# Performance work log

Hardware: AMD Instinct MI355X
Metric: run time of the kernel (lower is better)

Reference implementation:

```python
import jax, jax.numpy as jnp
import numpy as np

D, H, F, E, K = 1024, 16, 2048, 8, 2
EPS = 1e-5


def layernorm(x, g, b):
    m = jnp.mean(x, axis=-1, keepdims=True)
    v = jnp.mean((x - m) ** 2, axis=-1, keepdims=True)
    return (x - m) * jax.lax.rsqrt(v + EPS) * g + b


def mha(q_in, k_in, v_in, wq, wk, wv, bq, bk, bv, wo, bo):
    B, Tq, Dm = q_in.shape
    Tk = k_in.shape[1]
    dh = Dm // H
    q = (q_in @ wq + bq).reshape(B, Tq, H, dh)
    k = (k_in @ wk + bk).reshape(B, Tk, H, dh)
    v = (v_in @ wv + bv).reshape(B, Tk, H, dh)
    scores = jnp.einsum('bqhd,bkhd->bhqk', q, k) / jnp.sqrt(jnp.asarray(dh, q.dtype))
    attn = jax.nn.softmax(scores, axis=-1)
    out = jnp.einsum('bhqk,bkhd->bqhd', attn, v).reshape(B, Tq, Dm)
    return out @ wo + bo


def moe(x, rw, rb, w1, b1, w2, b2):
    B, T, Dm = x.shape
    xt = x.reshape(-1, Dm)                      # [N, D]
    N = xt.shape[0]
    logits = xt @ rw + rb                       # [N, E]
    probs = jax.nn.softmax(logits, axis=-1)
    topv, topi = jax.lax.top_k(probs, K)        # [N, K]
    gates = topv / jnp.sum(topv, axis=-1, keepdims=True)
    dense_gates = jnp.zeros((N, E), x.dtype).at[jnp.arange(N)[:, None], topi].set(gates)
    h = jax.nn.relu(jnp.einsum('td,edf->etf', xt, w1) + b1[:, None, :])  # [E, N, F]
    y = jnp.einsum('etf,efd->etd', h, w2) + b2[:, None, :]               # [E, N, D]
    out = jnp.einsum('te,etd->td', dense_gates, y).reshape(B, T, Dm)
    frac = jnp.mean(jnp.sum(jax.nn.one_hot(topi, E, dtype=x.dtype), axis=1) / K, axis=0)  # [E]
    importance = jnp.mean(probs, axis=0)        # [E]
    lb_loss = E * jnp.sum(frac * importance)
    return out, lb_loss


def forward(tgt, memory,
            sa_wq, sa_wk, sa_wv, sa_bq, sa_bk, sa_bv, sa_wo, sa_bo,
            ca_wq, ca_wk, ca_wv, ca_bq, ca_bk, ca_bv, ca_wo, ca_bo,
            ln1_g, ln1_b, ln2_g, ln2_b, ln3_g, ln3_b,
            rw, rb, w1, b1, w2, b2):
    t2 = mha(tgt, tgt, tgt, sa_wq, sa_wk, sa_wv, sa_bq, sa_bk, sa_bv, sa_wo, sa_bo)
    t = layernorm(tgt + t2, ln1_g, ln1_b)
    t2 = mha(t, memory, memory, ca_wq, ca_wk, ca_wv, ca_bq, ca_bk, ca_bv, ca_wo, ca_bo)
    t = layernorm(t + t2, ln2_g, ln2_b)
    t2, lb = moe(t, rw, rb, w1, b1, w2, b2)
    t = layernorm(t + t2, ln3_g, ln3_b)
    return t, lb


def setup_inputs() -> dict:
    key = jax.random.key(0)
    ks = jax.random.split(key, 24)
    s = 1.0 / np.sqrt(D)
    inp = {
        'tgt': jax.random.normal(ks[0], (4, 512, D), jnp.float32),
        'memory': jax.random.normal(ks[1], (4, 512, D), jnp.float32),
    }
    names = ['sa_wq', 'sa_wk', 'sa_wv', 'sa_wo', 'ca_wq', 'ca_wk', 'ca_wv', 'ca_wo']
    for i, n in enumerate(names):
        inp[n] = jax.random.normal(ks[2 + i], (D, D), jnp.float32) * s
    for n in ['sa_bq', 'sa_bk', 'sa_bv', 'sa_bo', 'ca_bq', 'ca_bk', 'ca_bv', 'ca_bo']:
        inp[n] = jnp.zeros((D,), jnp.float32)
    for n in ['ln1_g', 'ln2_g', 'ln3_g']:
        inp[n] = jnp.ones((D,), jnp.float32)
    for n in ['ln1_b', 'ln2_b', 'ln3_b']:
        inp[n] = jnp.zeros((D,), jnp.float32)
    inp['rw'] = jax.random.normal(ks[10], (D, E), jnp.float32) * s
    inp['rb'] = jnp.zeros((E,), jnp.float32)
    inp['w1'] = jax.random.normal(ks[11], (E, D, F), jnp.float32) * s
    inp['b1'] = jnp.zeros((E, F), jnp.float32)
    inp['w2'] = jax.random.normal(ks[12], (E, F, D), jnp.float32) * (1.0 / np.sqrt(F))
    inp['b2'] = jnp.zeros((E, D), jnp.float32)
    return inp


def reference(tgt, memory,
              sa_wq, sa_wk, sa_wv, sa_bq, sa_bk, sa_bv, sa_wo, sa_bo,
              ca_wq, ca_wk, ca_wv, ca_bq, ca_bk, ca_bv, ca_wo, ca_bo,
              ln1_g, ln1_b, ln2_g, ln2_b, ln3_g, ln3_b,
              rw, rb, w1, b1, w2, b2):
    return forward(tgt, memory,
                   sa_wq, sa_wk, sa_wv, sa_bq, sa_bk, sa_bv, sa_wo, sa_bo,
                   ca_wq, ca_wk, ca_wv, ca_bq, ca_bk, ca_bv, ca_wo, ca_bo,
                   ln1_g, ln1_b, ln2_g, ln2_b, ln3_g, ln3_b,
                   rw, rb, w1, b1, w2, b2)
```

## Files before the change

kernel.cpp:

```cpp
#include <hip/hip_runtime.h>

constexpr int Dm = 1024;
constexpr int NH = 16;
constexpr int Ff = 2048;
constexpr int NE = 8;
constexpr int Bn = 4;
constexpr int Tn = 512;
constexpr int Nt = 2048;

typedef float  f32x4  __attribute__((ext_vector_type(4)));
typedef __bf16 bf16x8 __attribute__((ext_vector_type(8)));
typedef unsigned short u16;
typedef u16 u16x8v __attribute__((ext_vector_type(8)));
typedef u16 u16x4v __attribute__((ext_vector_type(4)));

__device__ inline u16 f2bf(float f) {
    unsigned u = __builtin_bit_cast(unsigned, f);
    u += 0x7FFFu + ((u >> 16) & 1u);
    return (u16)(u >> 16);
}
__device__ inline float bf2f(u16 h) {
    unsigned u = (unsigned)h << 16;
    return __builtin_bit_cast(float, u);
}
__device__ inline void splitbf(float x, u16& hi, u16& lo) {
    hi = f2bf(x);
    lo = f2bf(x - bf2f(hi));
}
__device__ inline bf16x8 ld_frag(const u16* p) {
    return __builtin_bit_cast(bf16x8, *(const u16x8v*)p);
}
__device__ inline void cp16(const u16* g, u16* l) {
    __builtin_amdgcn_global_load_lds(
        (const __attribute__((address_space(1))) unsigned int*)g,
        (__attribute__((address_space(3))) unsigned int*)l, 16, 0, 0);
}

template <int SPLIT, int CMODE>
__global__ __launch_bounds__(256) void gemm_kernel(
    const u16* __restrict__ Ahi, const u16* __restrict__ Alo, int lda,
    const u16* __restrict__ Whi, const u16* __restrict__ Wlo, size_t weStride,
    const float* __restrict__ B0, const float* __restrict__ B1,
    const float* __restrict__ B2, size_t beStride,
    void* __restrict__ C0, void* __restrict__ C1, int ldc,
    int Mparam, int K,
    const int* __restrict__ lst, int lstStride, const int* __restrict__ cnt,
    int mode, int relu,
    const u16* __restrict__ A2hi, const u16* __restrict__ A2lo, int lda2,
    const u16* __restrict__ W2hi, const u16* __restrict__ W2lo,
    const float* __restrict__ B20, const float* __restrict__ B21,
    void* __restrict__ C20, void* __restrict__ C21, int ldc2, int xSplit,
    const float* __restrict__ gatep, float* __restrict__ accOut)
{
    __shared__ __align__(16) u16 AsH[128 * 32];
    __shared__ __align__(16) u16 WsH[128 * 32];
    __shared__ __align__(16) u16 AsL[SPLIT ? 128 * 32 : 8];
    __shared__ __align__(16) u16 WsL[SPLIT ? 128 * 32 : 8];
    __shared__ int inIdx[128];
    __shared__ int outIdx[128];

    const int e = blockIdx.z;
    const int M = (mode == 0) ? Mparam : cnt[e];
    const int m0 = blockIdx.y * 128;
    if (m0 >= M) return;

    int bx = blockIdx.x;
    const u16 *aH = Ahi, *aL = Alo, *wH = Whi, *wL = Wlo;
    const float *b0 = B0, *b1 = B1, *b2 = B2;
    void *c0 = C0, *c1 = C1;
    int myLda = lda, myLdc = ldc;
    if (xSplit && bx >= xSplit) {
        bx -= xSplit;
        aH = A2hi; aL = A2lo; wH = W2hi; wL = W2lo;
        b0 = B20; b1 = B21; b2 = B21;
        c0 = C20; c1 = C21; myLda = lda2; myLdc = ldc2;
    }
    const int n0 = bx * 128;
    const int seg = n0 >> 10, nseg = n0 & 1023;
    const float* bias = ((seg == 0) ? b0 : (seg == 1) ? b1 : b2) + (size_t)e * beStride;
    const int tid = threadIdx.x;

    if (tid < 128) {
        int g = m0 + tid;
        bool valid = g < M;
        int gi, go;
        if (mode == 0) { gi = valid ? g : (M - 1); go = valid ? g : -1; }
        else {
            int pid = lst[(size_t)e * lstStride + (valid ? g : 0)];
            gi = (mode == 1) ? (pid >> 1) : pid;
            go = valid ? pid : -1;
        }
        inIdx[tid] = gi;
        outIdx[tid] = go;
    }
    __syncthreads();

    const int lane = tid & 63, wv = tid >> 6;
    const int c0i = wv * 2, c1i = wv * 2 + 1;
    const int r0 = c0i * 16 + (lane >> 2), r1 = c1i * 16 + (lane >> 2);
    const int kc0 = (lane & 3) ^ ((r0 >> 1) & 3);
    const int kc1 = (lane & 3) ^ ((r1 >> 1) & 3);
    const size_t wOff = (size_t)e * weStride;
    const u16* aH0 = aH + (size_t)inIdx[r0] * myLda + kc0 * 8;
    const u16* aH1 = aH + (size_t)inIdx[r1] * myLda + kc1 * 8;
    const u16* wH0 = wH + wOff + (size_t)(n0 + r0) * K + kc0 * 8;
    const u16* wH1 = wH + wOff + (size_t)(n0 + r1) * K + kc1 * 8;
    const u16 *aL0 = nullptr, *aL1 = nullptr, *wL0 = nullptr, *wL1 = nullptr;
    if (SPLIT) {
        aL0 = aL + (size_t)inIdx[r0] * myLda + kc0 * 8;
        aL1 = aL + (size_t)inIdx[r1] * myLda + kc1 * 8;
        wL0 = wL + wOff + (size_t)(n0 + r0) * K + kc0 * 8;
        wL1 = wL + wOff + (size_t)(n0 + r1) * K + kc1 * 8;
    }
    u16* ldsA0 = &AsH[c0i * 512];
    u16* ldsA1 = &AsH[c1i * 512];
    u16* ldsW0 = &WsH[c0i * 512];
    u16* ldsW1 = &WsH[c1i * 512];
    u16* ldsAL0 = SPLIT ? &AsL[c0i * 512] : nullptr;
    u16* ldsAL1 = SPLIT ? &AsL[c1i * 512] : nullptr;
    u16* ldsWL0 = SPLIT ? &WsL[c0i * 512] : nullptr;
    u16* ldsWL1 = SPLIT ? &WsL[c1i * 512] : nullptr;

    const int wy = (wv >> 1) * 64, wx = (wv & 1) * 64;
    const int l15 = lane & 15, quad = lane >> 4;

    f32x4 acc[4][4];
    #pragma unroll
    for (int i = 0; i < 4; ++i)
        #pragma unroll
        for (int j = 0; j < 4; ++j) acc[i][j] = (f32x4)0.f;

    for (int k0 = 0; k0 < K; k0 += 32) {
        cp16(aH0 + k0, ldsA0);
        cp16(aH1 + k0, ldsA1);
        cp16(wH0 + k0, ldsW0);
        cp16(wH1 + k0, ldsW1);
        if (SPLIT) {
            cp16(aL0 + k0, ldsAL0);
            cp16(aL1 + k0, ldsAL1);
            cp16(wL0 + k0, ldsWL0);
            cp16(wL1 + k0, ldsWL1);
        }
        __syncthreads();

        bf16x8 ah[4], bh[4], al[4], bl[4];
        #pragma unroll
        for (int mi = 0; mi < 4; ++mi) {
            int r = wy + mi * 16 + l15;
            int sl = quad ^ ((r >> 1) & 3);
            ah[mi] = ld_frag(&AsH[r * 32 + sl * 8]);
            if (SPLIT) al[mi] = ld_frag(&AsL[r * 32 + sl * 8]);
        }
        #pragma unroll
        for (int ni = 0; ni < 4; ++ni) {
            int r = wx + ni * 16 + l15;
            int sl = quad ^ ((r >> 1) & 3);
            bh[ni] = ld_frag(&WsH[r * 32 + sl * 8]);
            if (SPLIT) bl[ni] = ld_frag(&WsL[r * 32 + sl * 8]);
        }
        #pragma unroll
        for (int mi = 0; mi < 4; ++mi)
            #pragma unroll
            for (int ni = 0; ni < 4; ++ni) {
                acc[mi][ni] = __builtin_amdgcn_mfma_f32_16x16x32_bf16(
                    ah[mi], bh[ni], acc[mi][ni], 0, 0, 0);
                if (SPLIT) {
                    acc[mi][ni] = __builtin_amdgcn_mfma_f32_16x16x32_bf16(
                        ah[mi], bl[ni], acc[mi][ni], 0, 0, 0);
                    acc[mi][ni] = __builtin_amdgcn_mfma_f32_16x16x32_bf16(
                        al[mi], bh[ni], acc[mi][ni], 0, 0, 0);
                }
            }
        __syncthreads();
    }

    #pragma unroll
    for (int mi = 0; mi < 4; ++mi) {
        #pragma unroll
        for (int r = 0; r < 4; ++r) {
            int rl = wy + mi * 16 + quad * 4 + r;
            int orow = outIdx[rl];
            if (orow < 0) continue;
            #pragma unroll
            for (int ni = 0; ni < 4; ++ni) {
                int col = nseg + wx + ni * 16 + l15;
                float val = acc[mi][ni][r] + bias[col];
                if (relu) val = fmaxf(val, 0.f);
                int gcol = n0 + wx + ni * 16 + l15;
                if (CMODE == 3) {
                    atomicAdd(&accOut[(size_t)(orow >> 1) * Dm + gcol],
                              gatep[orow] * val);
                } else if (CMODE == 2) {
                    u16 hh, ll;
                    splitbf(val, hh, ll);
                    ((u16*)c0)[(size_t)orow * myLdc + gcol] = hh;
                    ((u16*)c1)[(size_t)orow * myLdc + gcol] = ll;
                } else if (CMODE == 1) {
                    ((u16*)c0)[(size_t)orow * myLdc + gcol] = f2bf(val);
                } else {
                    ((float*)c0)[(size_t)orow * myLdc + gcol] = val;
                }
            }
        }
    }
}

__global__ __launch_bounds__(256) void attn_kernel(
    const u16* __restrict__ QH, const u16* __restrict__ QL, int qld, int qOff,
    const u16* __restrict__ KH, const u16* __restrict__ KL, int kld, int kOff,
    const u16* __restrict__ VH, const u16* __restrict__ VL, int vld, int vOff,
    u16* __restrict__ OH, u16* __restrict__ OL)
{
    __shared__ __align__(16) u16 KtH[64 * 72], KtL[64 * 72];
    __shared__ __align__(16) u16 VtH[64 * 72], VtL[64 * 72];
    __shared__ __align__(16) u16 PtH[4][16 * 72], PtL[4][16 * 72];

    const int tid = threadIdx.x, lane = tid & 63, wv = tid >> 6;
    const int quad = lane >> 4, l15 = lane & 15;
    const int b = blockIdx.z, h = blockIdx.y, q0 = blockIdx.x * 64;
    const int bT = b * Tn;

    bf16x8 aqh[2], aql[2];
    {
        size_t qbase = (size_t)(bT + q0 + wv * 16 + l15) * qld + qOff + h * 64;
        #pragma unroll
        for (int s = 0; s < 2; ++s) {
            aqh[s] = ld_frag(QH + qbase + s * 32 + quad * 8);
            aql[s] = ld_frag(QL + qbase + s * 32 + quad * 8);
        }
    }

    f32x4 oacc[4];
    #pragma unroll
    for (int i = 0; i < 4; ++i) oacc[i] = (f32x4)0.f;
    float mrow[4] = {-1e30f, -1e30f, -1e30f, -1e30f};
    float lrow[4] = {0.f, 0.f, 0.f, 0.f};

    const int rr = tid >> 2, cc = tid & 3;

    for (int kt0 = 0; kt0 < Tn; kt0 += 64) {
        {
            size_t kb = (size_t)(bT + kt0 + rr) * kld + kOff + h * 64 + cc * 16;
            *(u16x8v*)&KtH[rr * 72 + cc * 16]     = *(const u16x8v*)(KH + kb);
            *(u16x8v*)&KtH[rr * 72 + cc * 16 + 8] = *(const u16x8v*)(KH + kb + 8);
            *(u16x8v*)&KtL[rr * 72 + cc * 16]     = *(const u16x8v*)(KL + kb);
            *(u16x8v*)&KtL[rr * 72 + cc * 16 + 8] = *(const u16x8v*)(KL + kb + 8);

            size_t vb = (size_t)(bT + kt0 + rr) * vld + vOff + h * 64 + cc * 16;
            u16x8v va = *(const u16x8v*)(VH + vb);
            u16x8v vbv = *(const u16x8v*)(VH + vb + 8);
            u16x8v la = *(const u16x8v*)(VL + vb);
            u16x8v lb = *(const u16x8v*)(VL + vb + 8);
            #pragma unroll
            for (int i = 0; i < 8; ++i) {
                VtH[(cc * 16 + i) * 72 + rr]     = va[i];
                VtH[(cc * 16 + 8 + i) * 72 + rr] = vbv[i];
                VtL[(cc * 16 + i) * 72 + rr]     = la[i];
                VtL[(cc * 16 + 8 + i) * 72 + rr] = lb[i];
            }
        }
        __syncthreads();

        f32x4 sacc[4];
        #pragma unroll
        for (int nt = 0; nt < 4; ++nt) {
            sacc[nt] = (f32x4)0.f;
            #pragma unroll
            for (int s = 0; s < 2; ++s) {
                bf16x8 bkh = ld_frag(&KtH[(nt * 16 + l15) * 72 + s * 32 + quad * 8]);
                bf16x8 bkl = ld_frag(&KtL[(nt * 16 + l15) * 72 + s * 32 + quad * 8]);
                sacc[nt] = __builtin_amdgcn_mfma_f32_16x16x32_bf16(aqh[s], bkh, sacc[nt], 0, 0, 0);
                sacc[nt] = __builtin_amdgcn_mfma_f32_16x16x32_bf16(aqh[s], bkl, sacc[nt], 0, 0, 0);
                sacc[nt] = __builtin_amdgcn_mfma_f32_16x16x32_bf16(aql[s], bkh, sacc[nt], 0, 0, 0);
            }
        }
        #pragma unroll
        for (int nt = 0; nt < 4; ++nt)
            #pragma unroll
            for (int r = 0; r < 4; ++r) sacc[nt][r] *= 0.125f;

        float alpha[4], mnew[4];
        #pragma unroll
        for (int r = 0; r < 4; ++r) {
            float mx = fmaxf(fmaxf(sacc[0][r], sacc[1][r]), fmaxf(sacc[2][r], sacc[3][r]));
            #pragma unroll
            for (int msk = 1; msk < 16; msk <<= 1) mx = fmaxf(mx, __shfl_xor(mx, msk));
            mnew[r] = fmaxf(mrow[r], mx);
            alpha[r] = __expf(mrow[r] - mnew[r]);
            mrow[r] = mnew[r];
        }
        float rs[4] = {0.f, 0.f, 0.f, 0.f};
        #pragma unroll
        for (int nt = 0; nt < 4; ++nt)
            #pragma unroll
            for (int r = 0; r < 4; ++r) {
                float p = __expf(sacc[nt][r] - mnew[r]);
                sacc[nt][r] = p;
                rs[r] += p;
            }
        #pragma unroll
        for (int r = 0; r < 4; ++r) {
            #pragma unroll
            for (int msk = 1; msk < 16; msk <<= 1) rs[r] += __shfl_xor(rs[r], msk);
            lrow[r] = lrow[r] * alpha[r] + rs[r];
        }
        #pragma unroll
        for (int ni = 0; ni < 4; ++ni)
            #pragma unroll
            for (int r = 0; r < 4; ++r) oacc[ni][r] *= alpha[r];

        #pragma unroll
        for (int nt = 0; nt < 4; ++nt)
            #pragma unroll
            for (int r = 0; r < 4; ++r) {
                u16 hh, ll;
                splitbf(sacc[nt][r], hh, ll);
                PtH[wv][(quad * 4 + r) * 72 + nt * 16 + l15] = hh;
                PtL[wv][(quad * 4 + r) * 72 + nt * 16 + l15] = ll;
            }
        asm volatile("s_waitcnt lgkmcnt(0)" ::: "memory");

        #pragma unroll
        for (int s = 0; s < 2; ++s) {
            bf16x8 aph = ld_frag(&PtH[wv][l15 * 72 + s * 32 + quad * 8]);
            bf16x8 apl = ld_frag(&PtL[wv][l15 * 72 + s * 32 + quad * 8]);
            #pragma unroll
            for (int ni = 0; ni < 4; ++ni) {
                bf16x8 bvh = ld_frag(&VtH[(ni * 16 + l15) * 72 + s * 32 + quad * 8]);
                bf16x8 bvl = ld_frag(&VtL[(ni * 16 + l15) * 72 + s * 32 + quad * 8]);
                oacc[ni] = __builtin_amdgcn_mfma_f32_16x16x32_bf16(aph, bvh, oacc[ni], 0, 0, 0);
                oacc[ni] = __builtin_amdgcn_mfma_f32_16x16x32_bf16(aph, bvl, oacc[ni], 0, 0, 0);
                oacc[ni] = __builtin_amdgcn_mfma_f32_16x16x32_bf16(apl, bvh, oacc[ni], 0, 0, 0);
            }
        }
        __syncthreads();
    }

    #pragma unroll
    for (int r = 0; r < 4; ++r) {
        float inv = 1.f / lrow[r];
        int orow = bT + q0 + wv * 16 + quad * 4 + r;
        #pragma unroll
        for (int ni = 0; ni < 4; ++ni) {
            int col = h * 64 + ni * 16 + l15;
            u16 hh, ll;
            splitbf(oacc[ni][r] * inv, hh, ll);
            OH[(size_t)orow * Dm + col] = hh;
            OL[(size_t)orow * Dm + col] = ll;
        }
    }
}

__global__ __launch_bounds__(256) void ln_residual_kernel(
    const float* __restrict__ X, const float* __restrict__ R,
    const float* __restrict__ g, const float* __restrict__ bta,
    float* __restrict__ Out, u16* __restrict__ outH, u16* __restrict__ outL)
{
    __shared__ float red[8];
    const int t = blockIdx.x, tid = threadIdx.x;
    float v[4];
    float s = 0.f;
    #pragma unroll
    for (int i = 0; i < 4; ++i) {
        int c = tid + i * 256;
        v[i] = X[(size_t)t * Dm + c] + R[(size_t)t * Dm + c];
        s += v[i];
    }
    #pragma unroll
    for (int off = 32; off; off >>= 1) s += __shfl_down(s, off);
    const int wid = tid >> 6;
    if ((tid & 63) == 0) red[wid] = s;
    __syncthreads();
    const float mean = (red[0] + red[1] + red[2] + red[3]) * (1.f / 1024.f);
    float s2 = 0.f;
    #pragma unroll
    for (int i = 0; i < 4; ++i) { float d = v[i] - mean; s2 += d * d; }
    #pragma unroll
    for (int off = 32; off; off >>= 1) s2 += __shfl_down(s2, off);
    if ((tid & 63) == 0) red[4 + wid] = s2;
    __syncthreads();
    const float var  = (red[4] + red[5] + red[6] + red[7]) * (1.f / 1024.f);
    const float rstd = rsqrtf(var + 1e-5f);
    #pragma unroll
    for (int i = 0; i < 4; ++i) {
        int c = tid + i * 256;
        float o = (v[i] - mean) * rstd * g[c] + bta[c];
        Out[(size_t)t * Dm + c] = o;
        if (outH) {
            u16 hh, ll;
            splitbf(o, hh, ll);
            outH[(size_t)t * Dm + c] = hh;
            outL[(size_t)t * Dm + c] = ll;
        }
    }
}

__global__ __launch_bounds__(256) void split_kernel(
    const float* __restrict__ src, u16* __restrict__ hi, u16* __restrict__ lo)
{
    int i = (blockIdx.x * 256 + threadIdx.x) * 4;
    float4 v = *(const float4*)(src + i);
    u16x4v h, l;
    u16 hh, ll;
    splitbf(v.x, hh, ll); h[0] = hh; l[0] = ll;
    splitbf(v.y, hh, ll); h[1] = hh; l[1] = ll;
    splitbf(v.z, hh, ll); h[2] = hh; l[2] = ll;
    splitbf(v.w, hh, ll); h[3] = hh; l[3] = ll;
    *(u16x4v*)(hi + i) = h;
    *(u16x4v*)(lo + i) = l;
}

__global__ __launch_bounds__(256) void wT_kernel(
    const float* __restrict__ src, size_t srcEStride, int Ksrc, int Nsrc,
    u16* __restrict__ dhi, u16* __restrict__ dlo, size_t dstEStride)
{
    __shared__ float tile[64][65];
    const int e = blockIdx.z;
    src += (size_t)e * srcEStride;
    dhi += (size_t)e * dstEStride;
    if (dlo) dlo += (size_t)e * dstEStride;
    const int n0 = blockIdx.x * 64, k0 = blockIdx.y * 64;
    for (int i = threadIdx.x; i < 4096; i += 256) {
        int r = i >> 6, c = i & 63;
        tile[r][c] = src[(size_t)(k0 + r) * Nsrc + n0 + c];
    }
    __syncthreads();
    for (int i = threadIdx.x; i < 4096; i += 256) {
        int r = i >> 6, c = i & 63;
        float v = tile[c][r];
        u16 hh, ll;
        splitbf(v, hh, ll);
        dhi[(size_t)(n0 + r) * Ksrc + k0 + c] = hh;
        if (dlo) dlo[(size_t)(n0 + r) * Ksrc + k0 + c] = ll;
    }
}

constexpr int RT_TPB = 32;
__global__ __launch_bounds__(256) void router_kernel(
    const float* __restrict__ X, const float* __restrict__ rw,
    const float* __restrict__ rb, float* __restrict__ gatep,
    int* __restrict__ elist, int* __restrict__ ecnt,
    float* __restrict__ impf, float* __restrict__ cntf)
{
    __shared__ float simp[NE];
    __shared__ int   scnt[NE];
    __shared__ int   sbase[NE];
    __shared__ int   sexp[RT_TPB][2];
    __shared__ int   spos[RT_TPB][2];

    const int tid = threadIdx.x, lane = tid & 63, wv = tid >> 6;
    if (tid < NE) { simp[tid] = 0.f; scnt[tid] = 0; }
    __syncthreads();

    const int t0 = blockIdx.x * RT_TPB;

    for (int i = 0; i < 8; ++i) {
        const int slot = wv * 8 + i;
        const int t = t0 + slot;
        float l[NE];
        #pragma unroll
        for (int e = 0; e < NE; ++e) l[e] = 0.f;
        #pragma unroll
        for (int j = 0; j < Dm / 64; ++j) {
            int d = lane + j * 64;
            float x = X[(size_t)t * Dm + d];
            #pragma unroll
            for (int e = 0; e < NE; ++e) l[e] += x * rw[d * NE + e];
        }
        #pragma unroll
        for (int e = 0; e < NE; ++e) {
            float vv = l[e];
            #pragma unroll
            for (int off = 32; off; off >>= 1) vv += __shfl_down(vv, off);
            l[e] = vv;
        }
        if (lane == 0) {
            float mx = -1e30f;
            #pragma unroll
            for (int e = 0; e < NE; ++e) { l[e] += rb[e]; mx = fmaxf(mx, l[e]); }
            float p[NE];
            float sum = 0.f;
            #pragma unroll
            for (int e = 0; e < NE; ++e) { p[e] = __expf(l[e] - mx); sum += p[e]; }
            const float inv = 1.f / sum;
            int e0 = 0, e1 = 0;
            float v0 = -1.f, v1 = -1.f;
            #pragma unroll
            for (int e = 0; e < NE; ++e) {
                float pe = p[e] * inv;
                atomicAdd(&simp[e], pe);
                if (pe > v0)      { v1 = v0; e1 = e0; v0 = pe; e0 = e; }
                else if (pe > v1) { v1 = pe; e1 = e; }
            }
            const float gs = 1.f / (v0 + v1);
            sexp[slot][0] = e0;
            sexp[slot][1] = e1;
            spos[slot][0] = atomicAdd(&scnt[e0], 1);
            spos[slot][1] = atomicAdd(&scnt[e1], 1);
            gatep[2 * t]     = v0 * gs;
            gatep[2 * t + 1] = v1 * gs;
        }
    }
    __syncthreads();

    if (tid < NE) {
        sbase[tid] = atomicAdd(&ecnt[tid], scnt[tid]);
        atomicAdd(&impf[tid], simp[tid]);
        atomicAdd(&cntf[tid], (float)scnt[tid]);
    }
    __syncthreads();

    if (tid < RT_TPB * 2) {
        const int slot = tid >> 1, k = tid & 1;
        const int e = sexp[slot][k];
        elist[e * Nt + sbase[e] + spos[slot][k]] = 2 * (t0 + slot) + k;
    }
}

__global__ __launch_bounds__(256) void zero_kernel(
    float* __restrict__ t2, int* __restrict__ ecnt,
    float* __restrict__ impf, float* __restrict__ cntf)
{
    int i = blockIdx.x * 256 + threadIdx.x;
    *(float4*)&t2[(size_t)i * 4] = make_float4(0.f, 0.f, 0.f, 0.f);
    if (blockIdx.x == 0 && threadIdx.x < NE) {
        ecnt[threadIdx.x] = 0;
        impf[threadIdx.x] = 0.f;
        cntf[threadIdx.x] = 0.f;
    }
}

__global__ void lb_kernel(const float* __restrict__ impf,
                          const float* __restrict__ cntf,
                          float* __restrict__ out)
{
    if (threadIdx.x == 0) {
        float s = 0.f;
        for (int e = 0; e < NE; ++e) s += cntf[e] * impf[e];
        out[0] = (float)NE * s / ((float)Nt * 2.f * (float)Nt);
    }
}

extern "C" void kernel_launch(void* const* d_in, const int* in_sizes, int n_in,
                              void* d_out, int out_size, void* d_ws, size_t ws_size,
                              hipStream_t stream)
{
    const float* tgt   = (const float*)d_in[0];
    const float* memry = (const float*)d_in[1];
    const float* sa_wq = (const float*)d_in[2];
    const float* sa_wk = (const float*)d_in[3];
    const float* sa_wv = (const float*)d_in[4];
    const float* sa_wo = (const float*)d_in[5];
    const float* ca_wq = (const float*)d_in[6];
    const float* ca_wk = (const float*)d_in[7];
    const float* ca_wv = (const float*)d_in[8];
    const float* ca_wo = (const float*)d_in[9];
    const float* sa_bq = (const float*)d_in[10];
    const float* sa_bk = (const float*)d_in[11];
    const float* sa_bv = (const float*)d_in[12];
    const float* sa_bo = (const float*)d_in[13];
    const float* ca_bq = (const float*)d_in[14];
    const float* ca_bk = (const float*)d_in[15];
    const float* ca_bv = (const float*)d_in[16];
    const float* ca_bo = (const float*)d_in[17];
    const float* ln1_g = (const float*)d_in[18];
    const float* ln2_g = (const float*)d_in[19];
    const float* ln3_g = (const float*)d_in[20];
    const float* ln1_b = (const float*)d_in[21];
    const float* ln2_b = (const float*)d_in[22];
    const float* ln3_b = (const float*)d_in[23];
    const float* rw    = (const float*)d_in[24];
    const float* rb    = (const float*)d_in[25];
    const float* w1    = (const float*)d_in[26];
    const float* b1    = (const float*)d_in[27];
    const float* w2    = (const float*)d_in[28];
    const float* b2    = (const float*)d_in[29];

    const size_t ND = (size_t)Nt * Dm;
    const size_t MM = (size_t)1024 * 1024;
    u16* U = (u16*)d_ws;
    size_t off = 0;
    auto A = [&](size_t n) { u16* p = U + off; off += n; return p; };
    u16* qkvT_h  = A(3 * MM);  u16* qkvT_l  = A(3 * MM);
    u16* cakvT_h = A(2 * MM);  u16* cakvT_l = A(2 * MM);
    u16* caqT_h  = A(MM);      u16* caqT_l  = A(MM);
    u16* saoT_h  = A(MM);      u16* saoT_l  = A(MM);
    u16* caoT_h  = A(MM);      u16* caoT_l  = A(MM);
    u16* w1t     = A(16 * MM);
    u16* w2t     = A(16 * MM);
    u16* tgtH = A(ND);  u16* tgtL = A(ND);
    u16* memH = A(ND);  u16* memL = A(ND);
    u16* qkvH = A(3 * ND);  u16* qkvL = A(3 * ND);
    u16* kvcH = A(2 * ND);  u16* kvcL = A(2 * ND);
    u16* tbH  = A(ND);  u16* tbL = A(ND);
    u16* qcH = tgtH, *qcL = tgtL;
    u16* aoH = memH, *aoL = memL;
    u16* hbuf = qkvH;
    float* Fp = (float*)(U + off);
    float* t2 = Fp;
    float* tb = Fp + ND;
    float* gatep = tb + ND;
    int*   elist = (int*)(gatep + 2 * Nt);
    int*   ecnt  = elist + NE * Nt;
    float* impf  = (float*)(ecnt + NE);
    float* cntf  = impf + NE;
    float* outp  = (float*)d_out;

    dim3 blk(256);
    dim3 attnGrid(Tn / 64, NH, Bn);
    dim3 wtG(16, 16, 1);

    split_kernel<<<ND / 1024, blk, 0, stream>>>(tgt, tgtH, tgtL);
    split_kernel<<<ND / 1024, blk, 0, stream>>>(memry, memH, memL);
    wT_kernel<<<wtG, blk, 0, stream>>>(sa_wq, 0, 1024, 1024, qkvT_h,          qkvT_l,          0);
    wT_kernel<<<wtG, blk, 0, stream>>>(sa_wk, 0, 1024, 1024, qkvT_h + MM,     qkvT_l + MM,     0);
    wT_kernel<<<wtG, blk, 0, stream>>>(sa_wv, 0, 1024, 1024, qkvT_h + 2 * MM, qkvT_l + 2 * MM, 0);
    wT_kernel<<<wtG, blk, 0, stream>>>(ca_wk, 0, 1024, 1024, cakvT_h,         cakvT_l,         0);
    wT_kernel<<<wtG, blk, 0, stream>>>(ca_wv, 0, 1024, 1024, cakvT_h + MM,    cakvT_l + MM,    0);
    wT_kernel<<<wtG, blk, 0, stream>>>(ca_wq, 0, 1024, 1024, caqT_h, caqT_l, 0);
    wT_kernel<<<wtG, blk, 0, stream>>>(sa_wo, 0, 1024, 1024, saoT_h, saoT_l, 0);
    wT_kernel<<<wtG, blk, 0, stream>>>(ca_wo, 0, 1024, 1024, caoT_h, caoT_l, 0);
    wT_kernel<<<dim3(32, 16, 8), blk, 0, stream>>>(w1, 2 * MM, 1024, 2048, w1t, nullptr, 2 * MM);
    wT_kernel<<<dim3(16, 32, 8), blk, 0, stream>>>(w2, 2 * MM, 2048, 1024, w2t, nullptr, 2 * MM);

    gemm_kernel<1, 2><<<dim3(40, 16, 1), blk, 0, stream>>>(
        tgtH, tgtL, 1024, qkvT_h, qkvT_l, 0, sa_bq, sa_bk, sa_bv, 0,
        qkvH, qkvL, 3072, Nt, 1024, nullptr, 0, nullptr, 0, 0,
        memH, memL, 1024, cakvT_h, cakvT_l, ca_bk, ca_bv,
        kvcH, kvcL, 2048, 24, nullptr, nullptr);
    attn_kernel<<<attnGrid, blk, 0, stream>>>(
        qkvH, qkvL, 3072, 0, qkvH, qkvL, 3072, 1024, qkvH, qkvL, 3072, 2048,
        aoH, aoL);
    gemm_kernel<1, 0><<<dim3(8, 16, 1), blk, 0, stream>>>(
        aoH, aoL, 1024, saoT_h, saoT_l, 0, sa_bo, sa_bo, sa_bo, 0,
        t2, nullptr, 1024, Nt, 1024, nullptr, 0, nullptr, 0, 0,
        nullptr, nullptr, 0, nullptr, nullptr, nullptr, nullptr,
        nullptr, nullptr, 0, 0, nullptr, nullptr);
    ln_residual_kernel<<<Nt, blk, 0, stream>>>(tgt, t2, ln1_g, ln1_b, tb, tbH, tbL);

    gemm_kernel<1, 2><<<dim3(8, 16, 1), blk, 0, stream>>>(
        tbH, tbL, 1024, caqT_h, caqT_l, 0, ca_bq, ca_bq, ca_bq, 0,
        qcH, qcL, 1024, Nt, 1024, nullptr, 0, nullptr, 0, 0,
        nullptr, nullptr, 0, nullptr, nullptr, nullptr, nullptr,
        nullptr, nullptr, 0, 0, nullptr, nullptr);
    attn_kernel<<<attnGrid, blk, 0, stream>>>(
        qcH, qcL, 1024, 0, kvcH, kvcL, 2048, 0, kvcH, kvcL, 2048, 1024,
        aoH, aoL);
    gemm_kernel<1, 0><<<dim3(8, 16, 1), blk, 0, stream>>>(
        aoH, aoL, 1024, caoT_h, caoT_l, 0, ca_bo, ca_bo, ca_bo, 0,
        t2, nullptr, 1024, Nt, 1024, nullptr, 0, nullptr, 0, 0,
        nullptr, nullptr, 0, nullptr, nullptr, nullptr, nullptr,
        nullptr, nullptr, 0, 0, nullptr, nullptr);
    ln_residual_kernel<<<Nt, blk, 0, stream>>>(tb, t2, ln2_g, ln2_b, tb, tbH, tbL);

    zero_kernel<<<(Nt * Dm) / 1024, blk, 0, stream>>>(t2, ecnt, impf, cntf);
    router_kernel<<<Nt / RT_TPB, blk, 0, stream>>>(tb, rw, rb, gatep, elist, ecnt, impf, cntf);
    gemm_kernel<0, 1><<<dim3(16, 16, 8), blk, 0, stream>>>(
        tbH, nullptr, 1024, w1t, nullptr, 2 * MM, b1, b1 + 1024, b1 + 1024, Ff,
        hbuf, nullptr, 2048, 0, 1024, elist, Nt, ecnt, 1, 1,
        nullptr, nullptr, 0, nullptr, nullptr, nullptr, nullptr,
        nullptr, nullptr, 0, 0, nullptr, nullptr);
    gemm_kernel<0, 3><<<dim3(8, 16, 8), blk, 0, stream>>>(
        hbuf, nullptr, 2048, w2t, nullptr, 2 * MM, b2, b2, b2, Dm,
        nullptr, nullptr, 1024, 0, 2048, elist, Nt, ecnt, 2, 0,
        nullptr, nullptr, 0, nullptr, nullptr, nullptr, nullptr,
        nullptr, nullptr, 0, 0, gatep, t2);
    ln_residual_kernel<<<Nt, blk, 0, stream>>>(tb, t2, ln3_g, ln3_b, outp, nullptr, nullptr);
    lb_kernel<<<1, 64, 0, stream>>>(impf, cntf, outp + ND);
}
```

Before: 790.3 us.

## Add split-K to small and MoE GEMMs with atomic fp32 accumulation

Adds split-K support to the GEMM kernel. Blocks along y now cover both an M tile and a K slice, and partial sums are combined with atomicAdd into a zeroed fp32 buffer, with bias added only by the first slice. This applies to the attention projections, the cross-attention Q projection and both MoE expert GEMMs. The first expert GEMM now writes fp32, and a separate pass applies ReLU and converts to bf16. The aim is to fill the GPU with more blocks for GEMMs whose 128-row tiling gave too few blocks, at the cost of extra zeroing, conversion passes, atomic traffic and a large fp32 intermediate.

```diff
diff --git a/kernel.cpp b/kernel.cpp
--- a/kernel.cpp
+++ b/kernel.cpp
@@ -43,7 +43,7 @@
     const float* __restrict__ B0, const float* __restrict__ B1,
     const float* __restrict__ B2, size_t beStride,
     void* __restrict__ C0, void* __restrict__ C1, int ldc,
-    int Mparam, int K,
+    int Mparam, int K, int yTiles, int kLen,
     const int* __restrict__ lst, int lstStride, const int* __restrict__ cnt,
     int mode, int relu,
     const u16* __restrict__ A2hi, const u16* __restrict__ A2lo, int lda2,
@@ -61,8 +61,12 @@
 
     const int e = blockIdx.z;
     const int M = (mode == 0) ? Mparam : cnt[e];
-    const int m0 = blockIdx.y * 128;
+    const int ky = blockIdx.y / yTiles;
+    const int my = blockIdx.y % yTiles;
+    const int m0 = my * 128;
     if (m0 >= M) return;
+    const int kStart = ky * kLen;
+    const int kEnd = kStart + kLen;
 
     int bx = blockIdx.x;
     const u16 *aH = Ahi, *aL = Alo, *wH = Whi, *wL = Wlo;
@@ -130,7 +134,7 @@
         #pragma unroll
         for (int j = 0; j < 4; ++j) acc[i][j] = (f32x4)0.f;
 
-    for (int k0 = 0; k0 < K; k0 += 32) {
+    for (int k0 = kStart; k0 < kEnd; k0 += 32) {
         cp16(aH0 + k0, ldsA0);
         cp16(aH1 + k0, ldsA1);
         cp16(wH0 + k0, ldsW0);
@@ -174,6 +178,7 @@
         __syncthreads();
     }
 
+    const bool addB = (ky == 0);
     #pragma unroll
     for (int mi = 0; mi < 4; ++mi) {
         #pragma unroll
@@ -184,10 +189,12 @@
             #pragma unroll
             for (int ni = 0; ni < 4; ++ni) {
                 int col = nseg + wx + ni * 16 + l15;
-                float val = acc[mi][ni][r] + bias[col];
+                float val = acc[mi][ni][r] + (addB ? bias[col] : 0.f);
                 if (relu) val = fmaxf(val, 0.f);
                 int gcol = n0 + wx + ni * 16 + l15;
-                if (CMODE == 3) {
+                if (CMODE == 4) {
+                    atomicAdd(&((float*)c0)[(size_t)orow * myLdc + gcol], val);
+                } else if (CMODE == 3) {
                     atomicAdd(&accOut[(size_t)(orow >> 1) * Dm + gcol],
                               gatep[orow] * val);
                 } else if (CMODE == 2) {
@@ -433,6 +440,25 @@
         dhi[(size_t)(n0 + r) * Ksrc + k0 + c] = hh;
         if (dlo) dlo[(size_t)(n0 + r) * Ksrc + k0 + c] = ll;
     }
+}
+
+__global__ __launch_bounds__(256) void zero_f32(float* __restrict__ p)
+{
+    int i = blockIdx.x * 256 + threadIdx.x;
+    *(float4*)&p[(size_t)i * 4] = make_float4(0.f, 0.f, 0.f, 0.f);
+}
+
+__global__ __launch_bounds__(256) void hconvert_kernel(
+    const float* __restrict__ H, u16* __restrict__ hb)
+{
+    int i = (blockIdx.x * 256 + threadIdx.x) * 4;
+    float4 v = *(const float4*)(H + i);
+    u16x4v o;
+    o[0] = f2bf(fmaxf(v.x, 0.f));
+    o[1] = f2bf(fmaxf(v.y, 0.f));
+    o[2] = f2bf(fmaxf(v.z, 0.f));
+    o[3] = f2bf(fmaxf(v.w, 0.f));
+    *(u16x4v*)(hb + i) = o;
 }
 
 constexpr int RT_TPB = 32;
@@ -588,14 +614,17 @@
     u16* caoT_h  = A(MM);      u16* caoT_l  = A(MM);
     u16* w1t     = A(16 * MM);
     u16* w2t     = A(16 * MM);
-    u16* tgtH = A(ND);  u16* tgtL = A(ND);
-    u16* memH = A(ND);  u16* memL = A(ND);
-    u16* qkvH = A(3 * ND);  u16* qkvL = A(3 * ND);
-    u16* kvcH = A(2 * ND);  u16* kvcL = A(2 * ND);
-    u16* tbH  = A(ND);  u16* tbL = A(ND);
+    u16* actBase = A(16 * ND);
+    u16* tgtH = actBase;            u16* tgtL = actBase + ND;
+    u16* memH = actBase + 2 * ND;   u16* memL = actBase + 3 * ND;
+    u16* qkvH = actBase + 4 * ND;   u16* qkvL = actBase + 7 * ND;
+    u16* kvcH = actBase + 10 * ND;  u16* kvcL = actBase + 12 * ND;
+    u16* tbH  = actBase + 14 * ND;  u16* tbL  = actBase + 15 * ND;
     u16* qcH = tgtH, *qcL = tgtL;
     u16* aoH = memH, *aoL = memL;
-    u16* hbuf = qkvH;
+    float* qcF  = (float*)qkvH;
+    float* Hf32 = (float*)actBase;
+    u16*   hbuf = kvcH;
     float* Fp = (float*)(U + off);
     float* t2 = Fp;
     float* tb = Fp + ND;
@@ -625,44 +654,50 @@
 
     gemm_kernel<1, 2><<<dim3(40, 16, 1), blk, 0, stream>>>(
         tgtH, tgtL, 1024, qkvT_h, qkvT_l, 0, sa_bq, sa_bk, sa_bv, 0,
-        qkvH, qkvL, 3072, Nt, 1024, nullptr, 0, nullptr, 0, 0,
+        qkvH, qkvL, 3072, Nt, 1024, 16, 1024, nullptr, 0, nullptr, 0, 0,
         memH, memL, 1024, cakvT_h, cakvT_l, ca_bk, ca_bv,
         kvcH, kvcL, 2048, 24, nullptr, nullptr);
     attn_kernel<<<attnGrid, blk, 0, stream>>>(
         qkvH, qkvL, 3072, 0, qkvH, qkvL, 3072, 1024, qkvH, qkvL, 3072, 2048,
         aoH, aoL);
-    gemm_kernel<1, 0><<<dim3(8, 16, 1), blk, 0, stream>>>(
+    zero_f32<<<(Nt * Dm) / 1024, blk, 0, stream>>>(t2);
+    gemm_kernel<1, 4><<<dim3(8, 64, 1), blk, 0, stream>>>(
         aoH, aoL, 1024, saoT_h, saoT_l, 0, sa_bo, sa_bo, sa_bo, 0,
-        t2, nullptr, 1024, Nt, 1024, nullptr, 0, nullptr, 0, 0,
+        t2, nullptr, 1024, Nt, 1024, 16, 256, nullptr, 0, nullptr, 0, 0,
         nullptr, nullptr, 0, nullptr, nullptr, nullptr, nullptr,
         nullptr, nullptr, 0, 0, nullptr, nullptr);
     ln_residual_kernel<<<Nt, blk, 0, stream>>>(tgt, t2, ln1_g, ln1_b, tb, tbH, tbL);
 
-    gemm_kernel<1, 2><<<dim3(8, 16, 1), blk, 0, stream>>>(
+    zero_f32<<<(Nt * Dm) / 1024, blk, 0, stream>>>(qcF);
+    gemm_kernel<1, 4><<<dim3(8, 64, 1), blk, 0, stream>>>(
         tbH, tbL, 1024, caqT_h, caqT_l, 0, ca_bq, ca_bq, ca_bq, 0,
-        qcH, qcL, 1024, Nt, 1024, nullptr, 0, nullptr, 0, 0,
+        qcF, nullptr, 1024, Nt, 1024, 16, 256, nullptr, 0, nullptr, 0, 0,
         nullptr, nullptr, 0, nullptr, nullptr, nullptr, nullptr,
         nullptr, nullptr, 0, 0, nullptr, nullptr);
+    split_kernel<<<ND / 1024, blk, 0, stream>>>(qcF, qcH, qcL);
     attn_kernel<<<attnGrid, blk, 0, stream>>>(
         qcH, qcL, 1024, 0, kvcH, kvcL, 2048, 0, kvcH, kvcL, 2048, 1024,
         aoH, aoL);
-    gemm_kernel<1, 0><<<dim3(8, 16, 1), blk, 0, stream>>>(
+    zero_f32<<<(Nt * Dm) / 1024, blk, 0, stream>>>(t2);
+    gemm_kernel<1, 4><<<dim3(8, 64, 1), blk, 0, stream>>>(
         aoH, aoL, 1024, caoT_h, caoT_l, 0, ca_bo, ca_bo, ca_bo, 0,
-        t2, nullptr, 1024, Nt, 1024, nullptr, 0, nullptr, 0, 0,
+        t2, nullptr, 1024, Nt, 1024, 16, 256, nullptr, 0, nullptr, 0, 0,
         nullptr, nullptr, 0, nullptr, nullptr, nullptr, nullptr,
         nullptr, nullptr, 0, 0, nullptr, nullptr);
     ln_residual_kernel<<<Nt, blk, 0, stream>>>(tb, t2, ln2_g, ln2_b, tb, tbH, tbL);
 
     zero_kernel<<<(Nt * Dm) / 1024, blk, 0, stream>>>(t2, ecnt, impf, cntf);
+    zero_f32<<<(4096 * (size_t)Ff) / 1024, blk, 0, stream>>>(Hf32);
     router_kernel<<<Nt / RT_TPB, blk, 0, stream>>>(tb, rw, rb, gatep, elist, ecnt, impf, cntf);
-    gemm_kernel<0, 1><<<dim3(16, 16, 8), blk, 0, stream>>>(
+    gemm_kernel<0, 4><<<dim3(16, 32, 8), blk, 0, stream>>>(
         tbH, nullptr, 1024, w1t, nullptr, 2 * MM, b1, b1 + 1024, b1 + 1024, Ff,
-        hbuf, nullptr, 2048, 0, 1024, elist, Nt, ecnt, 1, 1,
+        Hf32, nullptr, 2048, 0, 1024, 16, 512, elist, Nt, ecnt, 1, 0,
         nullptr, nullptr, 0, nullptr, nullptr, nullptr, nullptr,
         nullptr, nullptr, 0, 0, nullptr, nullptr);
-    gemm_kernel<0, 3><<<dim3(8, 16, 8), blk, 0, stream>>>(
+    hconvert_kernel<<<(4096 * (size_t)Ff) / 1024, blk, 0, stream>>>(Hf32, hbuf);
+    gemm_kernel<0, 3><<<dim3(8, 64, 8), blk, 0, stream>>>(
         hbuf, nullptr, 2048, w2t, nullptr, 2 * MM, b2, b2, b2, Dm,
-        nullptr, nullptr, 1024, 0, 2048, elist, Nt, ecnt, 2, 0,
+        nullptr, nullptr, 1024, 0, 2048, 16, 512, elist, Nt, ecnt, 2, 0,
         nullptr, nullptr, 0, nullptr, nullptr, nullptr, nullptr,
         nullptr, nullptr, 0, 0, gatep, t2);
     ln_residual_kernel<<<Nt, blk, 0, stream>>>(tb, t2, ln3_g, ln3_b, outp, nullptr, nullptr);
```

Result: slower. 861.3 us (+9.0%).
